# Performance work log

Hardware: AMD Instinct MI355X
Metric: run time of the kernel (lower is better)

Reference implementation:

```python
import jax, jax.numpy as jnp
import numpy as np
from jax import lax

B, L, D = 2, 4096, 2048
K, KQ, M, H = 32, 4, 8, 8  # H = D*expand // (K*M)
MEM = K * H              # 256
FLAT = K * H * M         # 2048
CONV_W = 4
DIM_SWIGLU = H * 3 * 2   # out_expand_factor=3 -> 48
N_DECAY = K - 4          # 28 decay heads, 4 anchor heads


def setup_inputs() -> dict:
    key = jax.random.key(0)
    ks = jax.random.split(key, 8)
    x = jax.random.normal(ks[0], (B, L, D), dtype=jnp.float32)
    W_mem = jax.random.normal(ks[1], (D, MEM + K), dtype=jnp.float32) / np.sqrt(D)
    conv_k = jax.random.normal(ks[2], (CONV_W, 1, MEM + K), dtype=jnp.float32) * 0.3
    W_q = jax.random.normal(ks[3], (D, KQ * H * M * 2), dtype=jnp.float32) / np.sqrt(D)
    theta = jnp.asarray(np.tile(np.geomspace(0.001, 3.0, M).reshape(1, 1, 1, 1, M),
                                (1, 1, K, H, 1)), dtype=jnp.float32)
    decay_slopes = jnp.asarray(np.log(np.expm1(np.geomspace(0.001, 0.1, N_DECAY))), dtype=jnp.float32)
    anchor_slopes = jnp.asarray(np.log(np.expm1(np.geomspace(0.01, 0.1, 4))), dtype=jnp.float32)
    score_scale = jnp.ones((K,), dtype=jnp.float32)
    g = np.sqrt(2.0 / (H + DIM_SWIGLU))
    W_re = jax.random.normal(ks[4], (K, H, DIM_SWIGLU), dtype=jnp.float32) * g
    W_im = jax.random.normal(ks[5], (K, H, DIM_SWIGLU), dtype=jnp.float32) * g
    norm_scale = jnp.ones((1, 1, K, H), dtype=jnp.float32)
    W_out = jax.random.normal(ks[6], (K * H * 3, D), dtype=jnp.float32) / np.sqrt(K * H * 3)
    return {"x": x, "W_mem": W_mem, "conv_k": conv_k, "W_q": W_q, "theta": theta,
            "decay_slopes": decay_slopes, "anchor_slopes": anchor_slopes,
            "score_scale": score_scale, "W_re": W_re, "W_im": W_im,
            "norm_scale": norm_scale, "W_out": W_out}


def _forward(x, W_mem, conv_k, W_q, theta, decay_slopes, anchor_slopes,
             score_scale, W_re, W_im, norm_scale, W_out):
    b, l, d = x.shape
    # memory branch: dense + causal depthwise conv
    z = x @ W_mem  # (b, l, MEM+K)
    z = lax.conv_general_dilated(z, conv_k, window_strides=(1,),
                                 padding=[(CONV_W - 1, 0)],
                                 dimension_numbers=('NHC', 'HIO', 'NHC'),
                                 feature_group_count=MEM + K)
    k_val = z[..., :MEM].reshape(b, l, K, H)
    s_raw = z[..., MEM:].reshape(b, l, K, 1)
    # query branch
    q = (x @ W_q).reshape(b, l, KQ, H, M, 2)
    q_re, q_im = q[..., 0], q[..., 1]
    # per-head time weights (decay heads look back from end, anchor heads from start)
    pos = jnp.arange(l, dtype=jnp.float32)
    slopes_d = jax.nn.softplus(decay_slopes).reshape(1, 1, -1, 1)
    slopes_a = jax.nn.softplus(anchor_slopes).reshape(1, 1, -1, 1)
    dist = jnp.maximum(jnp.float32(l - 1) - pos, 0.0)
    log_w = jnp.concatenate([-slopes_d * dist[None, :, None, None],
                             -slopes_a * pos[None, :, None, None]], axis=2)  # (1,l,K,1)
    log_p = jnp.clip(score_scale[None, None, :, None] * s_raw, -20.0, 20.0)
    p_w = jnp.exp(log_p + log_w)  # (b,l,K,1)
    # complex rotation of keys
    phi = k_val[..., None] * theta          # (b,l,K,H,M)
    re_k, im_k = jnp.cos(phi), jnp.sin(phi)
    pw5 = p_w[..., None]
    merged = jnp.concatenate([p_w.squeeze(-1),
                              (pw5 * re_k).reshape(b, l, FLAT),
                              (pw5 * im_k).reshape(b, l, FLAT)], axis=-1)
    cs = jnp.cumsum(merged, axis=1)
    den = cs[..., :K]                       # (b,l,K)
    num_re = cs[..., K:K + FLAT]
    num_im = cs[..., K + FLAT:]
    inv_den = 1.0 / jnp.maximum(den[..., None], 1e-4)  # (b,l,K,1)
    state_re = num_re.reshape(b, l, K, H, M) * inv_den[..., None]
    state_im = num_im.reshape(b, l, K, H, M) * inv_den[..., None]
    # GQA-style query repeat
    n_rep = K // KQ
    q_re = jnp.repeat(q_re, n_rep, axis=2)
    q_im = jnp.repeat(q_im, n_rep, axis=2)
    out_re = jnp.sum(state_re * q_re + state_im * q_im, axis=-1)  # (b,l,K,H)
    out_im = jnp.sum(state_im * q_re - state_re * q_im, axis=-1)
    out_re = out_re * norm_scale
    out_im = out_im * norm_scale
    y = jnp.einsum('blkh,khn->blkn', out_re, W_re) + jnp.einsum('blkh,khn->blkn', out_im, W_im)
    y_val, y_gate = jnp.split(y, 2, axis=-1)
    y = (y_val * jax.nn.silu(y_gate)).reshape(b, l, -1)
    return y @ W_out


def reference(x, W_mem, conv_k, W_q, theta, decay_slopes, anchor_slopes,
              score_scale, W_re, W_im, norm_scale, W_out):
    return _forward(x, W_mem, conv_k, W_q, theta, decay_slopes, anchor_slopes,
                    score_scale, W_re, W_im, norm_scale, W_out)
```

## Files before the change

kernel.cpp:

```cpp
#include <hip/hip_runtime.h>
#include <hip/hip_bf16.h>
#include <math.h>

#define BB 2
#define LL 4096
#define DD 2048
#define KK 32
#define MEM 256
#define CTOT 288
#define NQ 512
#define ZSTR 800
#define NPAD 896
#define FLAT 2048
#define CMERG 4128
#define CH 16
#define NCH 256
#define YDIM 768
#define BL (BB*LL)

typedef __attribute__((ext_vector_type(4))) float f32x4;
typedef __attribute__((ext_vector_type(8))) short bf16x8;
typedef __attribute__((ext_vector_type(8))) unsigned short u16x8;

__device__ inline unsigned short f2b(float v) {
    __hip_bfloat16 h = __float2bfloat16(v);
    return *reinterpret_cast<unsigned short*>(&h);
}
__device__ inline float b2f(unsigned short u) {
    __hip_bfloat16 h;
    *reinterpret_cast<unsigned short*>(&h) = u;
    return __bfloat162float(h);
}

__device__ inline void gload16(const void* g, void* l) {
    __builtin_amdgcn_global_load_lds(
        (const __attribute__((address_space(1))) unsigned int*)g,
        (__attribute__((address_space(3))) unsigned int*)l, 16, 0, 0);
}

template<int HH>
__device__ inline float bcast8(float v) {
    return __int_as_float(__builtin_amdgcn_ds_swizzle(__float_as_int(v), (HH << 5) | 0x18));
}

__device__ inline float fast_sigmoid_mul(float val, float g) {
    return val * __builtin_amdgcn_rcpf(1.f + __expf(-g));
}

__global__ __launch_bounds__(256) void cvt_x(const float* __restrict__ x,
                                             unsigned short* __restrict__ xb) {
    size_t i = ((size_t)blockIdx.x * 256 + threadIdx.x) * 8;
    float4 a = *(const float4*)&x[i];
    float4 b = *(const float4*)&x[i + 4];
    u16x8 o;
    o[0] = f2b(a.x); o[1] = f2b(a.y); o[2] = f2b(a.z); o[3] = f2b(a.w);
    o[4] = f2b(b.x); o[5] = f2b(b.y); o[6] = f2b(b.z); o[7] = f2b(b.w);
    *(u16x8*)&xb[i] = o;
}

__global__ __launch_bounds__(256) void prep_wb(const float* __restrict__ W_mem,
                                               const float* __restrict__ W_q,
                                               unsigned short* __restrict__ Wb) {
    int n = blockIdx.x;
    for (int k = threadIdx.x; k < DD; k += 256) {
        float v = 0.f;
        if (n < CTOT) v = W_mem[(size_t)k * CTOT + n];
        else if (n < ZSTR) v = W_q[(size_t)k * NQ + (n - CTOT)];
        Wb[(size_t)n * DD + k] = f2b(v);
    }
}

__global__ __launch_bounds__(256) void prep_wo(const float* __restrict__ W_out,
                                               unsigned short* __restrict__ Wo) {
    int n = blockIdx.x;
    for (int k = threadIdx.x; k < YDIM; k += 256) {
        Wo[(size_t)n * YDIM + k] = f2b(W_out[(size_t)k * DD + n]);
    }
}

template<bool CBF16>
__global__ __launch_bounds__(256) void gemm_mfma(const unsigned short* __restrict__ A,
                                                 const unsigned short* __restrict__ Bh_g,
                                                 void* __restrict__ Cout,
                                                 int Kd, int Nvalid, int Cstride) {
    __shared__ unsigned short As[2][4096];
    __shared__ unsigned short Bh[2][4096];
    int tid = threadIdx.x;
    int lane = tid & 63;
    int wave = tid >> 6;
    int wr = wave >> 1, wc = wave & 1;

    int nwg = gridDim.x * gridDim.y;
    int bid = blockIdx.y * gridDim.x + blockIdx.x;
    int cpx = nwg >> 3;
    int swz = (bid & 7) * cpx + (bid >> 3);
    int bx = swz % gridDim.x, by = swz / gridDim.x;
    int m0 = by * 128;
    int n0 = bx * 128;

    f32x4 acc[4][4];
#pragma unroll
    for (int i = 0; i < 4; ++i)
#pragma unroll
        for (int j = 0; j < 4; ++j) acc[i][j] = (f32x4){0.f, 0.f, 0.f, 0.f};

    int f0 = tid, f1 = 256 + tid;
    int row0 = f0 >> 2, ks0 = (f0 & 3) ^ ((row0 >> 1) & 3);
    int row1 = f1 >> 2, ks1 = (f1 & 3) ^ ((row1 >> 1) & 3);
    const unsigned short* ga0 = &A[(size_t)(m0 + row0) * Kd + ks0 * 8];
    const unsigned short* ga1 = &A[(size_t)(m0 + row1) * Kd + ks1 * 8];
    const unsigned short* gb0 = &Bh_g[(size_t)(n0 + row0) * Kd + ks0 * 8];
    const unsigned short* gb1 = &Bh_g[(size_t)(n0 + row1) * Kd + ks1 * 8];
    int l0 = (wave * 64) * 8;
    int l1 = (256 + wave * 64) * 8;

    int g = lane >> 4, rr = lane & 15;

#define STAGE(buf, koff) do {                                          \
        gload16(ga0 + (koff), &As[buf][l0]);                           \
        gload16(ga1 + (koff), &As[buf][l1]);                           \
        gload16(gb0 + (koff), &Bh[buf][l0]);                           \
        gload16(gb1 + (koff), &Bh[buf][l1]);                           \
    } while (0)

    STAGE(0, 0);
    __syncthreads();

    int nIter = Kd >> 5;
    int cur = 0;
    for (int it = 0; it < nIter; ++it) {
        if (it + 1 < nIter) STAGE(cur ^ 1, (it + 1) * 32);

        bf16x8 av[4], bhv[4];
#pragma unroll
        for (int i = 0; i < 4; ++i) {
            int ra = wr * 64 + i * 16 + rr;
            av[i] = *(const bf16x8*)&As[cur][ra * 32 + ((g ^ ((ra >> 1) & 3)) * 8)];
            int rb = wc * 64 + i * 16 + rr;
            bhv[i] = *(const bf16x8*)&Bh[cur][rb * 32 + ((g ^ ((rb >> 1) & 3)) * 8)];
        }
#pragma unroll
        for (int i = 0; i < 4; ++i)
#pragma unroll
            for (int j = 0; j < 4; ++j)
                acc[i][j] = __builtin_amdgcn_mfma_f32_16x16x32_bf16(av[i], bhv[j], acc[i][j], 0, 0, 0);

        __syncthreads();
        cur ^= 1;
    }
#undef STAGE

    int cg = lane >> 4, cr = lane & 15;
#pragma unroll
    for (int i = 0; i < 4; ++i)
#pragma unroll
        for (int j = 0; j < 4; ++j) {
            int colb = n0 + wc * 64 + j * 16 + cr;
            if (colb < Nvalid) {
#pragma unroll
                for (int r = 0; r < 4; ++r) {
                    int rowb = m0 + wr * 64 + i * 16 + cg * 4 + r;
                    if (CBF16)
                        ((unsigned short*)Cout)[(size_t)rowb * Cstride + colb] = f2b(acc[i][j][r]);
                    else
                        ((float*)Cout)[(size_t)rowb * Cstride + colb] = acc[i][j][r];
                }
            }
        }
}

__global__ __launch_bounds__(512, 2) void gemm256(const unsigned short* __restrict__ A,
                                                  const unsigned short* __restrict__ Bm,
                                                  float* __restrict__ C,
                                                  int Kd, int Cstride) {
    __shared__ __attribute__((aligned(16))) unsigned short As[2][16384];
    __shared__ __attribute__((aligned(16))) unsigned short Bs[2][16384];
    int tid = threadIdx.x;
    int lane = tid & 63, wave = tid >> 6;
    int wm = wave >> 2, wn = wave & 3;

    int nwg = gridDim.x * gridDim.y;
    int bid = blockIdx.y * gridDim.x + blockIdx.x;
    int cpx = nwg >> 3;
    int swz = (bid & 7) * cpx + (bid >> 3);
    int bx = swz % gridDim.x, by = swz / gridDim.x;
    int m0 = by * 256, n0 = bx * 256;

    f32x4 acc[8][4];
#pragma unroll
    for (int i = 0; i < 8; ++i)
#pragma unroll
        for (int j = 0; j < 4; ++j) acc[i][j] = (f32x4){0.f, 0.f, 0.f, 0.f};

    const unsigned short* pA[4];
    const unsigned short* pB[4];
    int ldsoff[4];
#pragma unroll
    for (int j = 0; j < 4; ++j) {
        int f = j * 512 + tid;
        int row = f >> 3, s = f & 7;
        int sg = s ^ (row & 7);
        pA[j] = A + (size_t)(m0 + row) * Kd + sg * 8;
        pB[j] = Bm + (size_t)(n0 + row) * Kd + sg * 8;
        ldsoff[j] = (j * 512 + wave * 64) * 8;
    }

    int rr = lane & 15, kg = lane >> 4;

#pragma unroll
    for (int j = 0; j < 4; ++j) gload16(pB[j], &Bs[0][ldsoff[j]]);
#pragma unroll
    for (int j = 0; j < 4; ++j) gload16(pA[j], &As[0][ldsoff[j]]);
    asm volatile("s_waitcnt vmcnt(0)" ::: "memory");
    __builtin_amdgcn_s_barrier();

    int nT = Kd >> 6;
    int cur = 0;

#define LDA(fr, t) ({ int ra_ = wm * 128 + (fr) * 16 + rr;                       \
        int sd_ = (t) * 4 + kg;                                                  \
        *(const bf16x8*)&As[cur][(ra_ * 8 + (sd_ ^ (ra_ & 7))) * 8]; })
#define LDB(fc, t) ({ int rb_ = wn * 64 + (fc) * 16 + rr;                        \
        int sd_ = (t) * 4 + kg;                                                  \
        *(const bf16x8*)&Bs[cur][(rb_ * 8 + (sd_ ^ (rb_ & 7))) * 8]; })

    for (int it = 0; it < nT; ++it) {
        int nxt = cur ^ 1;
        bool hn = (it + 1 < nT);
        int k0n = (it + 1) << 6;

        if (hn) {
#pragma unroll
            for (int j = 0; j < 4; ++j) gload16(pB[j] + k0n, &Bs[nxt][ldsoff[j]]);
#pragma unroll
            for (int j = 0; j < 4; ++j) gload16(pA[j] + k0n, &As[nxt][ldsoff[j]]);
        }

        bf16x8 bv[8];
#pragma unroll
        for (int j = 0; j < 4; ++j) { bv[2 * j] = LDB(j, 0); bv[2 * j + 1] = LDB(j, 1); }
#pragma unroll
        for (int i = 0; i < 8; ++i) {
            bf16x8 a0 = LDA(i, 0);
            bf16x8 a1 = LDA(i, 1);
#pragma unroll
            for (int j = 0; j < 4; ++j) {
                acc[i][j] = __builtin_amdgcn_mfma_f32_16x16x32_bf16(a0, bv[2 * j], acc[i][j], 0, 0, 0);
                acc[i][j] = __builtin_amdgcn_mfma_f32_16x16x32_bf16(a1, bv[2 * j + 1], acc[i][j], 0, 0, 0);
            }
        }

        asm volatile("s_waitcnt vmcnt(0)" ::: "memory");
        __builtin_amdgcn_s_barrier();
        cur = nxt;
    }
#undef LDA
#undef LDB

    int cg = lane >> 4;
#pragma unroll
    for (int i = 0; i < 8; ++i)
#pragma unroll
        for (int j = 0; j < 4; ++j) {
            int colb = n0 + wn * 64 + j * 16 + rr;
#pragma unroll
            for (int r = 0; r < 4; ++r) {
                int rowb = m0 + wm * 128 + i * 16 + cg * 4 + r;
                C[(size_t)rowb * Cstride + colb] = acc[i][j][r];
            }
        }
}

__global__ __launch_bounds__(256) void fused_partial(const unsigned short* __restrict__ zq,
                                                     const float* __restrict__ conv_k,
                                                     const float* __restrict__ theta,
                                                     const float* __restrict__ decay,
                                                     const float* __restrict__ anchor,
                                                     const float* __restrict__ sscale,
                                                     float* __restrict__ partials) {
    int chunk = blockIdx.x, b = blockIdx.y, t = threadIdx.x;
    int l0 = chunk * CH;
    __shared__ unsigned short zin[CH + 3][CTOT];

    for (int idx = t; idx < (CH + 3) * 36; idx += 256) {
        int r = idx / 36, c8 = (idx % 36) * 8;
        int l = l0 - 3 + r;
        u16x8 v = (u16x8)(0);
        if (l >= 0) v = *(const u16x8*)&zq[(size_t)(b * LL + l) * ZSTR + c8];
        *(u16x8*)&zin[r][c8] = v;
    }
    __syncthreads();

    int k = t >> 3;
    float cz0 = conv_k[t], cz1 = conv_k[CTOT + t], cz2 = conv_k[2 * CTOT + t], cz3 = conv_k[3 * CTOT + t];
    int sc = MEM + k;
    float cs0 = conv_k[sc], cs1 = conv_k[CTOT + sc], cs2 = conv_k[2 * CTOT + sc], cs3 = conv_k[3 * CTOT + sc];
    float xx = (k < KK - 4) ? decay[k] : anchor[k - (KK - 4)];
    float sp = (xx > 20.f) ? xx : log1pf(__expf(xx));
    float ss = sscale[k];
    float th[8];
#pragma unroll
    for (int m = 0; m < 8; ++m) th[m] = theta[t * 8 + m];
    float rs[8], is[8];
#pragma unroll
    for (int m = 0; m < 8; ++m) { rs[m] = 0.f; is[m] = 0.f; }
    float dsum = 0.f;

#pragma unroll 1
    for (int i = 0; i < CH; ++i) {
        float kv = b2f(zin[i][t]) * cz0 + b2f(zin[i + 1][t]) * cz1 +
                   b2f(zin[i + 2][t]) * cz2 + b2f(zin[i + 3][t]) * cz3;
        float s = b2f(zin[i][sc]) * cs0 + b2f(zin[i + 1][sc]) * cs1 +
                  b2f(zin[i + 2][sc]) * cs2 + b2f(zin[i + 3][sc]) * cs3;
        int l = l0 + i;
        float lw = (k < KK - 4) ? -sp * (float)(LL - 1 - l) : -sp * (float)l;
        float lp = fminf(fmaxf(ss * s, -20.f), 20.f);
        float p = __expf(lp + lw);
        dsum += p;
#pragma unroll
        for (int m = 0; m < 8; ++m) {
            float sn, cn;
            __sincosf(kv * th[m], &sn, &cn);
            rs[m] += p * cn;
            is[m] += p * sn;
        }
    }
    size_t base = ((size_t)b * NCH + chunk) * CMERG;
    *(f32x4*)&partials[base + KK + t * 8]            = (f32x4){rs[0], rs[1], rs[2], rs[3]};
    *(f32x4*)&partials[base + KK + t * 8 + 4]        = (f32x4){rs[4], rs[5], rs[6], rs[7]};
    *(f32x4*)&partials[base + KK + FLAT + t * 8]     = (f32x4){is[0], is[1], is[2], is[3]};
    *(f32x4*)&partials[base + KK + FLAT + t * 8 + 4] = (f32x4){is[4], is[5], is[6], is[7]};
    if ((t & 7) == 0) partials[base + k] = dsum;
}

__global__ __launch_bounds__(256) void scan_partials(float* __restrict__ partials) {
    int t = threadIdx.x;
    int cl = t & 15, j = t >> 4;
    int c = blockIdx.x * 16 + cl;
    int b = blockIdx.y;
    float v[16];
    float s = 0.f;
#pragma unroll
    for (int i = 0; i < 16; ++i) {
        v[i] = partials[((size_t)b * NCH + j * 16 + i) * CMERG + c];
        s += v[i];
    }
    __shared__ float sums[16][17];
    sums[j][cl] = s;
    __syncthreads();
    if (j == 0) {
        float run = 0.f;
#pragma unroll
        for (int jj = 0; jj < 16; ++jj) {
            float x = sums[jj][cl];
            sums[jj][cl] = run;
            run += x;
        }
    }
    __syncthreads();
    float run = sums[j][cl];
#pragma unroll
    for (int i = 0; i < 16; ++i) {
        float x = v[i];
        partials[((size_t)b * NCH + j * 16 + i) * CMERG + c] = run;
        run += x;
    }
}

__global__ __launch_bounds__(256) void fused_stage(const unsigned short* __restrict__ zq,
                                                   const float* __restrict__ conv_k,
                                                   const float* __restrict__ theta,
                                                   const float* __restrict__ decay,
                                                   const float* __restrict__ anchor,
                                                   const float* __restrict__ sscale,
                                                   const float* __restrict__ partials,
                                                   const float* __restrict__ W_re,
                                                   const float* __restrict__ W_im,
                                                   const float* __restrict__ nscale,
                                                   unsigned short* __restrict__ y_act) {
    int chunk = blockIdx.x, b = blockIdx.y, t = threadIdx.x;
    int l0 = chunk * CH;
    __shared__ unsigned short zin[CH + 3][CTOT];
    __shared__ unsigned short qall[CH][NQ];

    for (int idx = t; idx < (CH + 3) * 36; idx += 256) {
        int r = idx / 36, c8 = (idx % 36) * 8;
        int l = l0 - 3 + r;
        u16x8 v = (u16x8)(0);
        if (l >= 0) v = *(const u16x8*)&zq[(size_t)(b * LL + l) * ZSTR + c8];
        *(u16x8*)&zin[r][c8] = v;
    }
    for (int idx = t; idx < CH * (NQ / 8); idx += 256) {
        int i = idx >> 6, c8 = (idx & 63) * 8;
        *(u16x8*)&qall[i][c8] = *(const u16x8*)&zq[(size_t)(b * LL + l0 + i) * ZSTR + CTOT + c8];
    }
    __syncthreads();

    int k = t >> 3, h = t & 7, w = t >> 6;
    float cz0 = conv_k[t], cz1 = conv_k[CTOT + t], cz2 = conv_k[2 * CTOT + t], cz3 = conv_k[3 * CTOT + t];
    int sc = MEM + k;
    float cs0 = conv_k[sc], cs1 = conv_k[CTOT + sc], cs2 = conv_k[2 * CTOT + sc], cs3 = conv_k[3 * CTOT + sc];
    float xx = (k < KK - 4) ? decay[k] : anchor[k - (KK - 4)];
    float sp = (xx > 20.f) ? xx : log1pf(__expf(xx));
    float ss = sscale[k];
    float th[8];
#pragma unroll
    for (int m = 0; m < 8; ++m) th[m] = theta[t * 8 + m];
    float ns = nscale[t];
    int qb = w * 128 + h * 16;

    float wre[8][6], wim[8][6];
#pragma unroll
    for (int hh = 0; hh < 8; ++hh)
#pragma unroll
        for (int jj = 0; jj < 6; ++jj) {
            wre[hh][jj] = W_re[(k * 8 + hh) * 48 + h + 8 * jj];
            wim[hh][jj] = W_im[(k * 8 + hh) * 48 + h + 8 * jj];
        }

    size_t pbase = ((size_t)b * NCH + chunk) * CMERG;
    f32x4 r0 = *(const f32x4*)&partials[pbase + KK + t * 8];
    f32x4 r1 = *(const f32x4*)&partials[pbase + KK + t * 8 + 4];
    f32x4 i0 = *(const f32x4*)&partials[pbase + KK + FLAT + t * 8];
    f32x4 i1 = *(const f32x4*)&partials[pbase + KK + FLAT + t * 8 + 4];
    float rs[8] = {r0[0], r0[1], r0[2], r0[3], r1[0], r1[1], r1[2], r1[3]};
    float is[8] = {i0[0], i0[1], i0[2], i0[3], i1[0], i1[1], i1[2], i1[3]};
    float den = partials[pbase + k];

#pragma unroll 1
    for (int i = 0; i < CH; ++i) {
        float kv = b2f(zin[i][t]) * cz0 + b2f(zin[i + 1][t]) * cz1 +
                   b2f(zin[i + 2][t]) * cz2 + b2f(zin[i + 3][t]) * cz3;
        float s = b2f(zin[i][sc]) * cs0 + b2f(zin[i + 1][sc]) * cs1 +
                  b2f(zin[i + 2][sc]) * cs2 + b2f(zin[i + 3][sc]) * cs3;
        int l = l0 + i;
        float lw = (k < KK - 4) ? -sp * (float)(LL - 1 - l) : -sp * (float)l;
        float lp = fminf(fmaxf(ss * s, -20.f), 20.f);
        float p = __expf(lp + lw);
        den += p;
        float inv = __builtin_amdgcn_rcpf(fmaxf(den, 1e-4f));
#pragma unroll
        for (int m = 0; m < 8; ++m) {
            float sn, cn;
            __sincosf(kv * th[m], &sn, &cn);
            rs[m] += p * cn;
            is[m] += p * sn;
        }
        u16x8 qv0 = *(const u16x8*)&qall[i][qb];
        u16x8 qv1 = *(const u16x8*)&qall[i][qb + 8];
        float o_re = 0.f, o_im = 0.f;
#pragma unroll
        for (int m = 0; m < 8; ++m) {
            float sre = rs[m] * inv;
            float sim = is[m] * inv;
            float qre = b2f((unsigned short)((m < 4) ? qv0[2 * m] : qv1[2 * m - 8]));
            float qim = b2f((unsigned short)((m < 4) ? qv0[2 * m + 1] : qv1[2 * m - 7]));
            o_re += sre * qre + sim * qim;
            o_im += sim * qre - sre * qim;
        }
        o_re *= ns;
        o_im *= ns;

        float y0 = 0.f, y1 = 0.f, y2 = 0.f, y3 = 0.f, y4 = 0.f, y5 = 0.f;
#define EAPPLY(HH) { float br_ = bcast8<HH>(o_re); float bi_ = bcast8<HH>(o_im); \
        y0 += br_ * wre[HH][0] + bi_ * wim[HH][0]; \
        y1 += br_ * wre[HH][1] + bi_ * wim[HH][1]; \
        y2 += br_ * wre[HH][2] + bi_ * wim[HH][2]; \
        y3 += br_ * wre[HH][3] + bi_ * wim[HH][3]; \
        y4 += br_ * wre[HH][4] + bi_ * wim[HH][4]; \
        y5 += br_ * wre[HH][5] + bi_ * wim[HH][5]; }
        EAPPLY(0) EAPPLY(1) EAPPLY(2) EAPPLY(3)
        EAPPLY(4) EAPPLY(5) EAPPLY(6) EAPPLY(7)
#undef EAPPLY

        size_t ybase = (size_t)(b * LL + l) * YDIM + k * 24 + h;
        y_act[ybase]      = f2b(fast_sigmoid_mul(y0 * y3, y3));
        y_act[ybase + 8]  = f2b(fast_sigmoid_mul(y1 * y4, y4));
        y_act[ybase + 16] = f2b(fast_sigmoid_mul(y2 * y5, y5));
    }
}

extern "C" void kernel_launch(void* const* d_in, const int* in_sizes, int n_in,
                              void* d_out, int out_size, void* d_ws, size_t ws_size,
                              hipStream_t stream) {
    const float* x      = (const float*)d_in[0];
    const float* W_mem  = (const float*)d_in[1];
    const float* conv_k = (const float*)d_in[2];
    const float* W_q    = (const float*)d_in[3];
    const float* theta  = (const float*)d_in[4];
    const float* decay  = (const float*)d_in[5];
    const float* anchor = (const float*)d_in[6];
    const float* sscale = (const float*)d_in[7];
    const float* W_re   = (const float*)d_in[8];
    const float* W_im   = (const float*)d_in[9];
    const float* nscale = (const float*)d_in[10];
    const float* W_out  = (const float*)d_in[11];
    float* out = (float*)d_out;
    float* ws = (float*)d_ws;

    unsigned short* xb = (unsigned short*)out;
    unsigned short* Wb = (unsigned short*)(out + 8388608);
    unsigned short* zq = (unsigned short*)(out + 9306112);
    float* partials      = ws;
    unsigned short* yb   = (unsigned short*)(ws + 2113536);
    unsigned short* Wo   = (unsigned short*)(ws + 5259264);

    cvt_x<<<8192, 256, 0, stream>>>(x, xb);
    prep_wb<<<NPAD, 256, 0, stream>>>(W_mem, W_q, Wb);
    prep_wo<<<DD, 256, 0, stream>>>(W_out, Wo);

    gemm_mfma<true><<<dim3(NPAD / 128, BL / 128), 256, 0, stream>>>(
        xb, Wb, zq, DD, ZSTR, ZSTR);
    fused_partial<<<dim3(NCH, BB), 256, 0, stream>>>(zq, conv_k, theta, decay, anchor, sscale, partials);
    scan_partials<<<dim3(CMERG / 16, BB), 256, 0, stream>>>(partials);
    fused_stage<<<dim3(NCH, BB), 256, 0, stream>>>(zq, conv_k, theta, decay, anchor, sscale,
                                                   partials, W_re, W_im, nscale, yb);
    gemm256<<<dim3(DD / 256, BL / 256), 512, 0, stream>>>(yb, Wo, out, YDIM, DD);
}
```

Measured before the change: 161.8 us.

## Use four-buffer LDS ring with two-stage prefetch in both GEMMs

Both bf16 MFMA GEMMs switch from double buffering with a full wait and barrier after each K step to a four-slot LDS ring that prefetches two stages ahead. Partial `s_waitcnt vmcnt` counts let later stages keep loading while the current one is consumed, with a single barrier per iteration. The 256x256 GEMM also shrinks its K tile from 64 to 32 and changes its swizzle so the ring fits in the same LDS footprint. This hides global-load latency better, at the cost of more iterations for gemm256 and doubled LDS use for gemm_mfma, which may lower its occupancy.

Measured after the change: 161.4 us. About the same (-0.2%).

```diff
diff --git a/kernel.cpp b/kernel.cpp
--- a/kernel.cpp
+++ b/kernel.cpp
@@ -38,6 +38,12 @@
         (__attribute__((address_space(3))) unsigned int*)l, 16, 0, 0);
 }
 
+__device__ inline void wait_stage(int it, int nIter) {
+    if (it + 3 <= nIter) asm volatile("s_waitcnt vmcnt(8)" ::: "memory");
+    else if (it + 2 == nIter) asm volatile("s_waitcnt vmcnt(4)" ::: "memory");
+    else asm volatile("s_waitcnt vmcnt(0)" ::: "memory");
+}
+
 template<int HH>
 __device__ inline float bcast8(float v) {
     return __int_as_float(__builtin_amdgcn_ds_swizzle(__float_as_int(v), (HH << 5) | 0x18));
@@ -83,8 +89,8 @@
                                                  const unsigned short* __restrict__ Bh_g,
                                                  void* __restrict__ Cout,
                                                  int Kd, int Nvalid, int Cstride) {
-    __shared__ unsigned short As[2][4096];
-    __shared__ unsigned short Bh[2][4096];
+    __shared__ unsigned short As[4][4096];
+    __shared__ unsigned short Bh[4][4096];
     int tid = threadIdx.x;
     int lane = tid & 63;
     int wave = tid >> 6;
@@ -123,13 +129,15 @@
         gload16(gb1 + (koff), &Bh[buf][l1]);                           \
     } while (0)
 
+    int nIter = Kd >> 5;
     STAGE(0, 0);
-    __syncthreads();
-
-    int nIter = Kd >> 5;
-    int cur = 0;
+    STAGE(1, 32);
+
     for (int it = 0; it < nIter; ++it) {
-        if (it + 1 < nIter) STAGE(cur ^ 1, (it + 1) * 32);
+        int cur = it & 3;
+        if (it + 2 < nIter) STAGE((it + 2) & 3, (it + 2) * 32);
+        wait_stage(it, nIter);
+        __builtin_amdgcn_s_barrier();
 
         bf16x8 av[4], bhv[4];
 #pragma unroll
@@ -144,9 +152,6 @@
 #pragma unroll
             for (int j = 0; j < 4; ++j)
                 acc[i][j] = __builtin_amdgcn_mfma_f32_16x16x32_bf16(av[i], bhv[j], acc[i][j], 0, 0, 0);
-
-        __syncthreads();
-        cur ^= 1;
     }
 #undef STAGE
 
@@ -173,8 +178,8 @@
                                                   const unsigned short* __restrict__ Bm,
                                                   float* __restrict__ C,
                                                   int Kd, int Cstride) {
-    __shared__ __attribute__((aligned(16))) unsigned short As[2][16384];
-    __shared__ __attribute__((aligned(16))) unsigned short Bs[2][16384];
+    __shared__ __attribute__((aligned(16))) unsigned short As[4][8192];
+    __shared__ __attribute__((aligned(16))) unsigned short Bs[4][8192];
     int tid = threadIdx.x;
     int lane = tid & 63, wave = tid >> 6;
     int wm = wave >> 2, wn = wave & 3;
@@ -192,14 +197,14 @@
 #pragma unroll
         for (int j = 0; j < 4; ++j) acc[i][j] = (f32x4){0.f, 0.f, 0.f, 0.f};
 
-    const unsigned short* pA[4];
-    const unsigned short* pB[4];
-    int ldsoff[4];
-#pragma unroll
-    for (int j = 0; j < 4; ++j) {
+    const unsigned short* pA[2];
+    const unsigned short* pB[2];
+    int ldsoff[2];
+#pragma unroll
+    for (int j = 0; j < 2; ++j) {
         int f = j * 512 + tid;
-        int row = f >> 3, s = f & 7;
-        int sg = s ^ (row & 7);
+        int row = f >> 2, s = f & 3;
+        int sg = s ^ ((row >> 1) & 3);
         pA[j] = A + (size_t)(m0 + row) * Kd + sg * 8;
         pB[j] = Bm + (size_t)(n0 + row) * Kd + sg * 8;
         ldsoff[j] = (j * 512 + wave * 64) * 8;
@@ -207,55 +212,42 @@
 
     int rr = lane & 15, kg = lane >> 4;
 
-#pragma unroll
-    for (int j = 0; j < 4; ++j) gload16(pB[j], &Bs[0][ldsoff[j]]);
-#pragma unroll
-    for (int j = 0; j < 4; ++j) gload16(pA[j], &As[0][ldsoff[j]]);
-    asm volatile("s_waitcnt vmcnt(0)" ::: "memory");
-    __builtin_amdgcn_s_barrier();
-
-    int nT = Kd >> 6;
-    int cur = 0;
-
-#define LDA(fr, t) ({ int ra_ = wm * 128 + (fr) * 16 + rr;                       \
-        int sd_ = (t) * 4 + kg;                                                  \
-        *(const bf16x8*)&As[cur][(ra_ * 8 + (sd_ ^ (ra_ & 7))) * 8]; })
-#define LDB(fc, t) ({ int rb_ = wn * 64 + (fc) * 16 + rr;                        \
-        int sd_ = (t) * 4 + kg;                                                  \
-        *(const bf16x8*)&Bs[cur][(rb_ * 8 + (sd_ ^ (rb_ & 7))) * 8]; })
+#define STAGE(buf, koff) do {                                          \
+        gload16(pA[0] + (koff), &As[buf][ldsoff[0]]);                  \
+        gload16(pA[1] + (koff), &As[buf][ldsoff[1]]);                  \
+        gload16(pB[0] + (koff), &Bs[buf][ldsoff[0]]);                  \
+        gload16(pB[1] + (koff), &Bs[buf][ldsoff[1]]);                  \
+    } while (0)
+
+    int nT = Kd >> 5;
+    STAGE(0, 0);
+    STAGE(1, 32);
+
+#define LDA(fr) ({ int ra_ = wm * 128 + (fr) * 16 + rr;                          \
+        *(const bf16x8*)&As[cur][ra_ * 32 + ((kg ^ ((ra_ >> 1) & 3)) * 8)]; })
+#define LDB(fc) ({ int rb_ = wn * 64 + (fc) * 16 + rr;                           \
+        *(const bf16x8*)&Bs[cur][rb_ * 32 + ((kg ^ ((rb_ >> 1) & 3)) * 8)]; })
 
     for (int it = 0; it < nT; ++it) {
-        int nxt = cur ^ 1;
-        bool hn = (it + 1 < nT);
-        int k0n = (it + 1) << 6;
-
-        if (hn) {
-#pragma unroll
-            for (int j = 0; j < 4; ++j) gload16(pB[j] + k0n, &Bs[nxt][ldsoff[j]]);
-#pragma unroll
-            for (int j = 0; j < 4; ++j) gload16(pA[j] + k0n, &As[nxt][ldsoff[j]]);
-        }
-
-        bf16x8 bv[8];
-#pragma unroll
-        for (int j = 0; j < 4; ++j) { bv[2 * j] = LDB(j, 0); bv[2 * j + 1] = LDB(j, 1); }
+        int cur = it & 3;
+        if (it + 2 < nT) STAGE((it + 2) & 3, (it + 2) * 32);
+        wait_stage(it, nT);
+        __builtin_amdgcn_s_barrier();
+
+        bf16x8 bv[4];
+#pragma unroll
+        for (int j = 0; j < 4; ++j) bv[j] = LDB(j);
 #pragma unroll
         for (int i = 0; i < 8; ++i) {
-            bf16x8 a0 = LDA(i, 0);
-            bf16x8 a1 = LDA(i, 1);
-#pragma unroll
-            for (int j = 0; j < 4; ++j) {
-                acc[i][j] = __builtin_amdgcn_mfma_f32_16x16x32_bf16(a0, bv[2 * j], acc[i][j], 0, 0, 0);
-                acc[i][j] = __builtin_amdgcn_mfma_f32_16x16x32_bf16(a1, bv[2 * j + 1], acc[i][j], 0, 0, 0);
-            }
-        }
-
-        asm volatile("s_waitcnt vmcnt(0)" ::: "memory");
-        __builtin_amdgcn_s_barrier();
-        cur = nxt;
+            bf16x8 a0 = LDA(i);
+#pragma unroll
+            for (int j = 0; j < 4; ++j)
+                acc[i][j] = __builtin_amdgcn_mfma_f32_16x16x32_bf16(a0, bv[j], acc[i][j], 0, 0, 0);
+        }
     }
 #undef LDA
 #undef LDB
+#undef STAGE
 
     int cg = lane >> 4;
 #pragma unroll
```
